# Kernel tuning notes

Hardware: AMD Instinct MI355X
Metric: run time of the kernel (lower is better)

Reference implementation:

```python
import jax, jax.numpy as jnp
import numpy as np


def setup_inputs() -> dict:
    key = jax.random.key(0)
    k1, k2 = jax.random.split(key)
    B, H, W = 32, 512, 512
    F, KH, KW = 32, 3, 3
    x = jax.random.normal(k1, (B, H, W), dtype=jnp.float32)
    # TF TruncatedNormal(mean=0.5, stddev=0.05 default)
    kernel_w = 0.5 + 0.05 * jax.random.truncated_normal(k2, -2.0, 2.0, (F, KH, KW), dtype=jnp.float32)
    biases = jnp.zeros((F,), dtype=jnp.float32)
    return {"x": x, "kernel_w": kernel_w, "biases": biases}


def reference(x, kernel_w, biases):
    # Quantize inputs and weights (binarized/ternary-style)
    x_q = jnp.round(x)                                   # [B,H,W]
    k_q = jnp.clip(jnp.round(kernel_w), -1.0, 1.0)       # [F,KH,KW]
    # scipy convolve2d is true convolution -> flip kernel spatially
    k_flip = k_q[:, ::-1, ::-1]
    # [F,KH,KW] -> HWIO [KH,KW,1,F]
    w = jnp.transpose(k_flip, (1, 2, 0))[:, :, None, :]
    xb = x_q[..., None]                                  # NHWC with C=1
    out = jax.lax.conv_general_dilated(
        xb, w, window_strides=(1, 1), padding='VALID',
        dimension_numbers=('NHWC', 'HWIO', 'NHWC'))      # [B,H-2,W-2,F]
    out = out + jnp.round(biases)                        # rounded per-channel bias
    # training-phase activation (binarization >=0 is the inference branch)
    return jax.nn.relu(out)
```

## Files before the change

kernel.cpp:

```cpp
#include <hip/hip_runtime.h>


#define BATCH 32
#define H 512
#define W 512
#define NF 32
#define HO 510
#define WO 510

typedef float vfloat4 __attribute__((ext_vector_type(4)));

__global__ __launch_bounds__(256) void cwt_conv_kernel(
    const float* __restrict__ x,
    const float* __restrict__ kw,
    const float* __restrict__ bias,
    float* __restrict__ out)
{
    const int tid = threadIdx.x;
    const int f4  = tid & 7;
    const int jq  = tid >> 3;
    const int i   = blockIdx.x;
    const int b   = blockIdx.y;
    const int j0  = jq * 16;

    float wq[9][4];
    float bq[4];
#pragma unroll
    for (int c = 0; c < 4; ++c) {
        int f = f4 * 4 + c;
#pragma unroll
        for (int t = 0; t < 9; ++t) {
            float v = rintf(kw[f * 9 + (8 - t)]);
            wq[t][c] = fminf(fmaxf(v, -1.0f), 1.0f);
        }
        bq[c] = rintf(bias[f]);
    }

    const float* rp = x + ((size_t)(b * H + i) * W + j0);
    const bool tail = (jq != 31);
    float xr[3][18];
#pragma unroll
    for (int r = 0; r < 3; ++r) {
        const float* rr = rp + (size_t)r * W;
#pragma unroll
        for (int q = 0; q < 4; ++q) {
            const float4 v4 = *reinterpret_cast<const float4*>(rr + q * 4);
            xr[r][q * 4 + 0] = rintf(v4.x);
            xr[r][q * 4 + 1] = rintf(v4.y);
            xr[r][q * 4 + 2] = rintf(v4.z);
            xr[r][q * 4 + 3] = rintf(v4.w);
        }
        if (tail) {
            const float2 v2 = *reinterpret_cast<const float2*>(rr + 16);
            xr[r][16] = rintf(v2.x);
            xr[r][17] = rintf(v2.y);
        } else {
            xr[r][16] = 0.0f;
            xr[r][17] = 0.0f;
        }
    }

    vfloat4* out4 = reinterpret_cast<vfloat4*>(out);
    const int obase = ((b * HO + i) * WO + j0) * (NF / 4) + f4;

#pragma unroll
    for (int jj = 0; jj < 16; ++jj) {
        float a0 = bq[0], a1 = bq[1], a2 = bq[2], a3 = bq[3];
#pragma unroll
        for (int r = 0; r < 3; ++r) {
#pragma unroll
            for (int dj = 0; dj < 3; ++dj) {
                const float xv = xr[r][jj + dj];
                const int t = r * 3 + dj;
                a0 = fmaf(xv, wq[t][0], a0);
                a1 = fmaf(xv, wq[t][1], a1);
                a2 = fmaf(xv, wq[t][2], a2);
                a3 = fmaf(xv, wq[t][3], a3);
            }
        }
        if (j0 + jj < WO) {
            vfloat4 o;
            o.x = fmaxf(a0, 0.0f);
            o.y = fmaxf(a1, 0.0f);
            o.z = fmaxf(a2, 0.0f);
            o.w = fmaxf(a3, 0.0f);
            __builtin_nontemporal_store(o, &out4[obase + jj * (NF / 4)]);
        }
    }
}

extern "C" void kernel_launch(void* const* d_in, const int* in_sizes, int n_in,
                              void* d_out, int out_size, void* d_ws, size_t ws_size,
                              hipStream_t stream) {
    const float* x    = (const float*)d_in[0];
    const float* kw   = (const float*)d_in[1];
    const float* bias = (const float*)d_in[2];
    float* out = (float*)d_out;

    dim3 grid(HO, BATCH);
    dim3 block(256);
    cwt_conv_kernel<<<grid, block, 0, stream>>>(x, kw, bias, out);
}
```

Measured before the change: 1.066 ms.

## Stage input rows and quantized weights in LDS, interleave output columns per wave

Each block now cooperatively loads and rounds its three input rows into shared memory, and weights and biases are quantized once per block into shared memory instead of per thread. Each thread now handles 16 strided columns rather than 16 contiguous ones, so a wavefront's stores cover 8 consecutive output positions (1 KB contiguous) per step. This is meant to remove redundant global and weight loads and improve store coalescing. In exchange it adds LDS reads in the inner loop and a block barrier.

```diff
diff --git a/kernel.cpp b/kernel.cpp
--- a/kernel.cpp
+++ b/kernel.cpp
@@ -16,75 +16,81 @@
     const float* __restrict__ bias,
     float* __restrict__ out)
 {
+    __shared__ float xs[3][W];
+    __shared__ float ws[9][NF];
+    __shared__ float bs[NF];
+
     const int tid = threadIdx.x;
-    const int f4  = tid & 7;
-    const int jq  = tid >> 3;
-    const int i   = blockIdx.x;
-    const int b   = blockIdx.y;
-    const int j0  = jq * 16;
+    const int i = blockIdx.x;
+    const int b = blockIdx.y;
+
+    for (int idx = tid; idx < 9 * NF; idx += 256) {
+        const int t = idx >> 5;
+        const int f = idx & 31;
+        const float v = rintf(kw[f * 9 + (8 - t)]);
+        ws[t][f] = fminf(fmaxf(v, -1.0f), 1.0f);
+    }
+    if (tid < NF) bs[tid] = rintf(bias[tid]);
+
+    const float* xrow = x + ((size_t)(b * H + i)) * W;
+#pragma unroll
+    for (int k = 0; k < 2; ++k) {
+        const int idx = tid + k * 256;
+        if (idx < 384) {
+            const int r  = idx >> 7;
+            const int c4 = idx & 127;
+            const float4 v = reinterpret_cast<const float4*>(xrow + (size_t)r * W)[c4];
+            float* d = &xs[r][c4 * 4];
+            d[0] = rintf(v.x); d[1] = rintf(v.y);
+            d[2] = rintf(v.z); d[3] = rintf(v.w);
+        }
+    }
+    __syncthreads();
+
+    const int lane = tid & 63;
+    const int wv   = tid >> 6;
+    const int f4   = lane & 7;
+    const int jg   = lane >> 3;
 
     float wq[9][4];
+#pragma unroll
+    for (int t = 0; t < 9; ++t) {
+        const float4 w4 = *reinterpret_cast<const float4*>(&ws[t][f4 * 4]);
+        wq[t][0] = w4.x; wq[t][1] = w4.y; wq[t][2] = w4.z; wq[t][3] = w4.w;
+    }
     float bq[4];
-#pragma unroll
-    for (int c = 0; c < 4; ++c) {
-        int f = f4 * 4 + c;
-#pragma unroll
-        for (int t = 0; t < 9; ++t) {
-            float v = rintf(kw[f * 9 + (8 - t)]);
-            wq[t][c] = fminf(fmaxf(v, -1.0f), 1.0f);
-        }
-        bq[c] = rintf(bias[f]);
+    {
+        const float4 b4 = *reinterpret_cast<const float4*>(&bs[f4 * 4]);
+        bq[0] = b4.x; bq[1] = b4.y; bq[2] = b4.z; bq[3] = b4.w;
     }
 
-    const float* rp = x + ((size_t)(b * H + i) * W + j0);
-    const bool tail = (jq != 31);
-    float xr[3][18];
+    const int jbase = wv * 128 + jg;
+    vfloat4* out4 = reinterpret_cast<vfloat4*>(out);
+    const int obase = ((b * HO + i) * WO + jbase) * (NF / 4) + f4;
+
+#pragma unroll 4
+    for (int s = 0; s < 16; ++s) {
+        const int j = jbase + 8 * s;
+        if (j < WO) {
+            float a0 = bq[0], a1 = bq[1], a2 = bq[2], a3 = bq[3];
 #pragma unroll
-    for (int r = 0; r < 3; ++r) {
-        const float* rr = rp + (size_t)r * W;
+            for (int r = 0; r < 3; ++r) {
 #pragma unroll
-        for (int q = 0; q < 4; ++q) {
-            const float4 v4 = *reinterpret_cast<const float4*>(rr + q * 4);
-            xr[r][q * 4 + 0] = rintf(v4.x);
-            xr[r][q * 4 + 1] = rintf(v4.y);
-            xr[r][q * 4 + 2] = rintf(v4.z);
-            xr[r][q * 4 + 3] = rintf(v4.w);
-        }
-        if (tail) {
-            const float2 v2 = *reinterpret_cast<const float2*>(rr + 16);
-            xr[r][16] = rintf(v2.x);
-            xr[r][17] = rintf(v2.y);
-        } else {
-            xr[r][16] = 0.0f;
-            xr[r][17] = 0.0f;
-        }
-    }
-
-    vfloat4* out4 = reinterpret_cast<vfloat4*>(out);
-    const int obase = ((b * HO + i) * WO + j0) * (NF / 4) + f4;
-
-#pragma unroll
-    for (int jj = 0; jj < 16; ++jj) {
-        float a0 = bq[0], a1 = bq[1], a2 = bq[2], a3 = bq[3];
-#pragma unroll
-        for (int r = 0; r < 3; ++r) {
-#pragma unroll
-            for (int dj = 0; dj < 3; ++dj) {
-                const float xv = xr[r][jj + dj];
-                const int t = r * 3 + dj;
-                a0 = fmaf(xv, wq[t][0], a0);
-                a1 = fmaf(xv, wq[t][1], a1);
-                a2 = fmaf(xv, wq[t][2], a2);
-                a3 = fmaf(xv, wq[t][3], a3);
+                for (int dj = 0; dj < 3; ++dj) {
+                    const float xv = xs[r][j + dj];
+                    const int t = r * 3 + dj;
+                    a0 = fmaf(xv, wq[t][0], a0);
+                    a1 = fmaf(xv, wq[t][1], a1);
+                    a2 = fmaf(xv, wq[t][2], a2);
+                    a3 = fmaf(xv, wq[t][3], a3);
+                }
             }
-        }
-        if (j0 + jj < WO) {
             vfloat4 o;
             o.x = fmaxf(a0, 0.0f);
             o.y = fmaxf(a1, 0.0f);
             o.z = fmaxf(a2, 0.0f);
             o.w = fmaxf(a3, 0.0f);
-            __builtin_nontemporal_store(o, &out4[obase + jj * (NF / 4)]);
+            __builtin_nontemporal_store(o, &out4[obase + s * 8 * (NF / 4)]);
         }
     }
 }
```

Result: no change. 1.055 ms (-1.0%).
